# Performance work log

Hardware: AMD Instinct MI355X
Metric: run time of the kernel (lower is better)

## Reference

```python
import jax, jax.numpy as jnp
import numpy as np

D_MODEL = 1024
D_ATT = 1024
N_HEAD = 16
HEAD_DIM = D_ATT // N_HEAD


def setup_inputs() -> dict:
    key = jax.random.key(0)
    ks = jax.random.split(key, 9)
    s = 0.02
    return {
        "x": jax.random.normal(ks[0], (4, 2048, D_MODEL), dtype=jnp.float32),
        "Wq": jax.random.normal(ks[1], (D_MODEL, D_ATT), dtype=jnp.float32) * s,
        "bq": jnp.zeros((D_ATT,), dtype=jnp.float32),
        "Wk": jax.random.normal(ks[2], (D_MODEL, D_ATT), dtype=jnp.float32) * s,
        "bk": jnp.zeros((D_ATT,), dtype=jnp.float32),
        "Wv": jax.random.normal(ks[3], (D_MODEL, D_ATT), dtype=jnp.float32) * s,
        "bv": jnp.zeros((D_ATT,), dtype=jnp.float32),
        "Wp": jax.random.normal(ks[4], (D_ATT, D_MODEL), dtype=jnp.float32) * s,
        "bp": jnp.zeros((D_MODEL,), dtype=jnp.float32),
    }


def reference(x, Wq, bq, Wk, bk, Wv, bv, Wp, bp):
    B, T, C = x.shape
    # project and split heads: [B, H, T, Dh]
    q = (x @ Wq + bq).reshape(B, T, N_HEAD, HEAD_DIM).transpose(0, 2, 1, 3)
    k = (x @ Wk + bk).reshape(B, T, N_HEAD, HEAD_DIM).transpose(0, 2, 1, 3)
    v = (x @ Wv + bv).reshape(B, T, N_HEAD, HEAD_DIM).transpose(0, 2, 1, 3)
    scale = 1.0 / jnp.sqrt(jnp.float32(HEAD_DIM))
    att = jnp.einsum("bhqd,bhkd->bhqk", q, k) * scale
    causal = jnp.tril(jnp.ones((T, T), dtype=bool))
    att = jnp.where(causal, att, jnp.float32(-jnp.inf))
    att = jax.nn.softmax(att, axis=-1)
    y = jnp.einsum("bhqk,bhkd->bhqd", att, v)
    y = y.transpose(0, 2, 1, 3).reshape(B, T, D_ATT)
    return y @ Wp + bp
```

## Files before the change

kernel.cpp:

```cpp
#include <hip/hip_runtime.h>
#include <hip/hip_bf16.h>
#include <stdint.h>

#define TSEQ 2048
#define NB   4
#define NHEAD 16
#define HDIM 64
#define DM   1024
#define BTOT (NB*TSEQ)

typedef __attribute__((ext_vector_type(8))) short bf16x8;
typedef __attribute__((ext_vector_type(4))) float f32x4;
typedef __attribute__((ext_vector_type(16))) float f32x16;
typedef __attribute__((ext_vector_type(2))) unsigned u32x2;

__device__ __forceinline__ unsigned short f2bf(float f){
  union { float f; unsigned u; } v; v.f = f;
  unsigned r = v.u + 0x7fffu + ((v.u >> 16) & 1u);
  return (unsigned short)(r >> 16);
}

__device__ __forceinline__ unsigned cvt_pk_bf16(float lo, float hi){
  unsigned r;
  asm("v_cvt_pk_bf16_f32 %0, %1, %2" : "=v"(r) : "v"(lo), "v"(hi));
  return r;
}

__device__ __forceinline__ float exp2_raw(float x){
#if __has_builtin(__builtin_amdgcn_exp2f)
  return __builtin_amdgcn_exp2f(x);
#else
  return exp2f(x);
#endif
}

__device__ __forceinline__ u32x2 pl32swap(unsigned a, unsigned b){
  auto r = __builtin_amdgcn_permlane32_swap((int)a, (int)b, false, false);
  return (u32x2){(unsigned)r[0], (unsigned)r[1]};
}

__device__ __forceinline__ void gload_lds16(const void* g, void* l){
  __builtin_amdgcn_global_load_lds(
      (const __attribute__((address_space(1))) void*)g,
      (__attribute__((address_space(3))) void*)l,
      16, 0, 0);
}

__global__ __launch_bounds__(256) void k_prep(
    const float* __restrict__ x, unsigned short* __restrict__ x_bf,
    const float* __restrict__ Wq, const float* __restrict__ Wk,
    const float* __restrict__ Wv, const float* __restrict__ Wp,
    unsigned short* __restrict__ Wq_t, unsigned short* __restrict__ Wk_t,
    unsigned short* __restrict__ Wv_t, unsigned short* __restrict__ Wp_t)
{
  __shared__ unsigned short tile_s[32][33];
  const int bid = blockIdx.x;
  if (bid < 8192){
    size_t j = ((size_t)bid * 256 + threadIdx.x) * 4;
    float4 v = *reinterpret_cast<const float4*>(x + j);
    unsigned long long pk =  (unsigned long long)f2bf(v.x)
                          | ((unsigned long long)f2bf(v.y) << 16)
                          | ((unsigned long long)f2bf(v.z) << 32)
                          | ((unsigned long long)f2bf(v.w) << 48);
    *reinterpret_cast<unsigned long long*>(x_bf + j) = pk;
  } else {
    const int r   = bid - 8192;
    const int job = r >> 10, tile = r & 1023;
    const float* W = (job == 0) ? Wq : (job == 1) ? Wk : (job == 2) ? Wv : Wp;
    unsigned short* Wt = (job == 0) ? Wq_t : (job == 1) ? Wk_t : (job == 2) ? Wv_t : Wp_t;
    const int n0 = (tile & 31) * 32, k0 = (tile >> 5) * 32;
    const int tx = threadIdx.x & 31, ty = threadIdx.x >> 5;
    #pragma unroll
    for (int j = ty; j < 32; j += 8)
      tile_s[j][tx] = f2bf(W[(size_t)(k0 + j) * DM + n0 + tx]);
    __syncthreads();
    #pragma unroll
    for (int j = ty; j < 32; j += 8)
      Wt[(size_t)(n0 + j) * DM + k0 + tx] = tile_s[tx][j];
  }
}

template<int MODE, int BM, int BN, int WM, int WN>
__global__ __launch_bounds__(512) void k_gemm2(
    const unsigned short* __restrict__ A,
    const unsigned short* __restrict__ Bt,
    const float* __restrict__ bias,
    const float* __restrict__ bias2,
    void* __restrict__ out, int M, int N, int K, float oscale)
{
  constexpr int TM = BM / WM, TN = BN / WN;
  constexpr int MF = TM / 16, NF = TN / 16;
  constexpr int AH = BM / 2,  BH = BN / 2;
  __shared__ unsigned short As[2][2][AH * 64];
  __shared__ unsigned short Bs[2][2][BH * 64];

  const int t    = threadIdx.x;
  const int lane = t & 63;
  const int w    = t >> 6;
  const int wm   = w / WN;
  const int wn   = w % WN;
  const int lr   = lane & 15;
  const int ck   = lane >> 4;
  const int rb   = ck << 2;

  const int gx  = gridDim.x;
  const int nwg = gx * gridDim.y;
  const int lid = blockIdx.y * gx + blockIdx.x;
  const int swz = (lid & 7) * (nwg >> 3) + (lid >> 3);
  const int n0  = (swz % gx) * BN;
  const int m0  = (swz / gx) * BM;

  const int aHalf = (wm * TM) / AH, aBase = (wm * TM) % AH;
  const int bHalf = (wn * TN) / BH, bBase = (wn * TN) % BH;

  auto stgA = [&](int buf, int kt){
    #pragma unroll
    for (int ht = 0; ht < 2; ++ht)
      #pragma unroll
      for (int rr = 0; rr < AH / 64; ++rr){
        int u = t + rr * 512;
        int row = u >> 3, c = u & 7, cs = c ^ (row & 7);
        gload_lds16(A + (size_t)(m0 + ht * AH + row) * K + kt * 64 + cs * 8,
                    &As[buf][ht][u * 8]);
      }
  };
  auto stgB = [&](int buf, int kt){
    #pragma unroll
    for (int ht = 0; ht < 2; ++ht)
      #pragma unroll
      for (int rr = 0; rr < BH / 64; ++rr){
        int u = t + rr * 512;
        int row = u >> 3, c = u & 7, cs = c ^ (row & 7);
        gload_lds16(Bt + (size_t)(n0 + ht * BH + row) * K + kt * 64 + cs * 8,
                    &Bs[buf][ht][u * 8]);
      }
  };

  f32x4 acc[MF][NF];
  #pragma unroll
  for (int i = 0; i < MF; ++i)
    #pragma unroll
    for (int j = 0; j < NF; ++j) acc[i][j] = (f32x4){0.f, 0.f, 0.f, 0.f};

  const int NT = K >> 6;

  stgA(0, 0); stgB(0, 0);

  for (int kt = 0; kt < NT; ++kt){
    const int cur = kt & 1;
    const unsigned short* Ah = &As[cur][aHalf][0];
    const unsigned short* Bh = &Bs[cur][bHalf][0];

    if (kt + 1 < NT){
      stgA(cur ^ 1, kt + 1);
      asm volatile("s_waitcnt vmcnt(%0)" :: "n"(BM / 64) : "memory");
    } else {
      asm volatile("s_waitcnt vmcnt(0)" ::: "memory");
    }
    __builtin_amdgcn_s_barrier();
    __builtin_amdgcn_sched_barrier(0);
    {
      bf16x8 af[MF], bfr[NF];
      #pragma unroll
      for (int i = 0; i < MF; ++i)
        af[i]  = *reinterpret_cast<const bf16x8*>(&Ah[(aBase + i * 16 + lr) * 64 + (ck ^ (lr & 7)) * 8]);
      #pragma unroll
      for (int i = 0; i < NF; ++i)
        bfr[i] = *reinterpret_cast<const bf16x8*>(&Bh[(bBase + i * 16 + lr) * 64 + (ck ^ (lr & 7)) * 8]);
      __builtin_amdgcn_s_setprio(1);
      #pragma unroll
      for (int mi = 0; mi < MF; ++mi)
        #pragma unroll
        for (int ni = 0; ni < NF; ++ni)
          acc[mi][ni] = __builtin_amdgcn_mfma_f32_16x16x32_bf16(af[mi], bfr[ni], acc[mi][ni], 0, 0, 0);
      __builtin_amdgcn_s_setprio(0);
    }

    if (kt + 1 < NT) stgB(cur ^ 1, kt + 1);
    {
      bf16x8 af[MF], bfr[NF];
      #pragma unroll
      for (int i = 0; i < MF; ++i)
        af[i]  = *reinterpret_cast<const bf16x8*>(&Ah[(aBase + i * 16 + lr) * 64 + ((4 + ck) ^ (lr & 7)) * 8]);
      #pragma unroll
      for (int i = 0; i < NF; ++i)
        bfr[i] = *reinterpret_cast<const bf16x8*>(&Bh[(bBase + i * 16 + lr) * 64 + ((4 + ck) ^ (lr & 7)) * 8]);
      __builtin_amdgcn_s_setprio(1);
      #pragma unroll
      for (int mi = 0; mi < MF; ++mi)
        #pragma unroll
        for (int ni = 0; ni < NF; ++ni)
          acc[mi][ni] = __builtin_amdgcn_mfma_f32_16x16x32_bf16(af[mi], bfr[ni], acc[mi][ni], 0, 0, 0);
      __builtin_amdgcn_s_setprio(0);
    }
    __builtin_amdgcn_s_barrier();
  }

  #pragma unroll
  for (int mf = 0; mf < MF; ++mf){
    #pragma unroll
    for (int ni = 0; ni < NF; ++ni){
      #pragma unroll
      for (int r = 0; r < 4; ++r){
        int m = m0 + wm * TM + mf * 16 + rb + r;
        int n = n0 + wn * TN + ni * 16 + lr;
        float v = acc[mf][ni][r];
        if (MODE == 1){
          v = (v + bias[m]) * oscale;
          int b = n >> 11, tt = n & 2047, h = m >> 6, d = m & 63;
          ((unsigned short*)out)[(((size_t)(b * 16 + h) * 64 + d) << 11) + tt] = f2bf(v);
        } else if (MODE == 2){
          v += bias[n];
          ((float*)out)[(size_t)m * N + n] = v;
        } else {
          int seg = n >> 10, nn = n & 1023;
          v += seg ? bias2[nn] : bias[nn];
          if (!seg) v *= oscale;
          int b = m >> 11, tt = m & 2047, h = nn >> 6, d = nn & 63;
          ((unsigned short*)out)[(size_t)seg * BTOT * DM +
              (((size_t)(b * 16 + h) * 2048 + tt) << 6) + d] = f2bf(v);
        }
      }
    }
  }
}

#define ATTN_PV(OD, KB)                                                        \
  {                                                                            \
    unsigned pk0a = cvt_pk_bf16(p[0],  p[1]);                                  \
    unsigned pk0b = cvt_pk_bf16(p[2],  p[3]);                                  \
    unsigned pk1a = cvt_pk_bf16(p[4],  p[5]);                                  \
    unsigned pk1b = cvt_pk_bf16(p[6],  p[7]);                                  \
    unsigned pk2a = cvt_pk_bf16(p[8],  p[9]);                                  \
    unsigned pk2b = cvt_pk_bf16(p[10], p[11]);                                 \
    unsigned pk3a = cvt_pk_bf16(p[12], p[13]);                                 \
    unsigned pk3b = cvt_pk_bf16(p[14], p[15]);                                 \
    __builtin_amdgcn_s_setprio(1);                                             \
    {                                                                          \
      u32x2 r0 = pl32swap(pk0a, pk1a);                                         \
      u32x2 r1 = pl32swap(pk0b, pk1b);                                         \
      union { unsigned u[4]; bf16x8 v; } ap;                                   \
      ap.u[0] = r0[0]; ap.u[1] = r1[0]; ap.u[2] = r0[1]; ap.u[3] = r1[1];      \
      const int wg = (KB) * 2;                                                 \
      _Pragma("unroll")                                                        \
      for (int ntd = 0; ntd < 2; ++ntd){                                       \
        int row = ntd * 32 + l31;                                              \
        bf16x8 bV = *reinterpret_cast<const bf16x8*>(                          \
            &Vs[cur][row * 64 + ((2 * wg + c2) ^ (row & 7)) * 8]);             \
        OD[ntd] = __builtin_amdgcn_mfma_f32_32x32x16_bf16(ap.v, bV, OD[ntd], 0, 0, 0); \
      }                                                                        \
    }                                                                          \
    {                                                                          \
      u32x2 r0 = pl32swap(pk2a, pk3a);                                         \
      u32x2 r1 = pl32swap(pk2b, pk3b);                                         \
      union { unsigned u[4]; bf16x8 v; } ap;                                   \
      ap.u[0] = r0[0]; ap.u[1] = r1[0]; ap.u[2] = r0[1]; ap.u[3] = r1[1];      \
      const int wg = (KB) * 2 + 1;                                             \
      _Pragma("unroll")                                                        \
      for (int ntd = 0; ntd < 2; ++ntd){                                       \
        int row = ntd * 32 + l31;                                              \
        bf16x8 bV = *reinterpret_cast<const bf16x8*>(                          \
            &Vs[cur][row * 64 + ((2 * wg + c2) ^ (row & 7)) * 8]);             \
        OD[ntd] = __builtin_amdgcn_mfma_f32_32x32x16_bf16(ap.v, bV, OD[ntd], 0, 0, 0); \
      }                                                                        \
    }                                                                          \
    __builtin_amdgcn_s_setprio(0);                                             \
  }

#define ATTN_SUBTILE(OD, KB)                                                   \
  {                                                                            \
    const int kvb = kv0 + (KB) * 32;                                           \
    if (kvb <= wave_max){                                                      \
      f32x16 st = {};                                                          \
      __builtin_amdgcn_s_setprio(1);                                           \
      _Pragma("unroll")                                                        \
      for (int m = 0; m < 4; ++m){                                             \
        int row = (KB) * 32 + l31;                                             \
        bf16x8 aK = *reinterpret_cast<const bf16x8*>(                          \
            &Ks[cur][row * 64 + ((2 * m + c2) ^ (row & 7)) * 8]);              \
        st = __builtin_amdgcn_mfma_f32_32x32x16_bf16(aK, bQ[m], st, 0, 0, 0);  \
      }                                                                        \
      __builtin_amdgcn_s_setprio(0);                                           \
      const bool need_mask = (kvb + 31 > q0);                                  \
      float p[16];                                                             \
      _Pragma("unroll")                                                        \
      for (int rg = 0; rg < 16; ++rg){                                         \
        float pv = exp2_raw(st[rg]);                                           \
        if (need_mask){                                                        \
          int kv = kvb + 4 * c2 + 8 * (rg >> 2) + (rg & 3);                    \
          pv = (kv > qrow) ? 0.f : pv;                                         \
        }                                                                      \
        p[rg] = pv;                                                            \
      }                                                                        \
      {                                                                        \
        float s0 = (p[0] + p[1]) + (p[2] + p[3]);                              \
        float s1 = (p[4] + p[5]) + (p[6] + p[7]);                              \
        float s2 = (p[8] + p[9]) + (p[10] + p[11]);                            \
        float s3 = (p[12] + p[13]) + (p[14] + p[15]);                          \
        l_part += (s0 + s1) + (s2 + s3);                                       \
      }                                                                        \
      ATTN_PV(OD, KB)                                                          \
    }                                                                          \
  }

__global__ __launch_bounds__(512) void k_attn(
    const unsigned short* __restrict__ Qb,
    const unsigned short* __restrict__ Kb,
    const unsigned short* __restrict__ Vt,
    unsigned short* __restrict__ Ya)
{
  __shared__ unsigned short Ks[2][64 * 64];
  __shared__ unsigned short Vs[2][64 * 64];

  const int t    = threadIdx.x;
  const int lane = t & 63;
  const int w    = t >> 6;
  const int bh   = blockIdx.y;
  const int blk  = blockIdx.x;
  const int l31  = lane & 31;
  const int c2   = lane >> 5;

  const unsigned short* Qp = Qb + (size_t)bh * TSEQ * 64;
  const unsigned short* Kp = Kb + (size_t)bh * TSEQ * 64;
  const unsigned short* Vp = Vt + (size_t)bh * 64 * TSEQ;
  const int b = bh >> 4, h = bh & 15;

  const int qt   = (w >> 2) ? (15 - blk) : blk;
  const int q0   = qt * 128 + (w & 3) * 32;
  const int wave_max = q0 + 31;
  const int ntiles   = 2 * (15 - blk) + 2;
  const int qrow = q0 + l31;

  auto stage = [&](int buf, int kv0){
    int row = t >> 3, c = t & 7;
    int cs = c ^ (row & 7);
    gload_lds16(Kp + (size_t)(kv0 + row) * 64 + cs * 8, &Ks[buf][t * 8]);
    gload_lds16(Vp + (size_t)row * TSEQ + kv0 + cs * 8, &Vs[buf][t * 8]);
  };

  bf16x8 bQ[4];
  #pragma unroll
  for (int m = 0; m < 4; ++m)
    bQ[m] = *reinterpret_cast<const bf16x8*>(
        Qp + (size_t)qrow * 64 + m * 16 + c2 * 8);

  f32x16 oA[2] = {}, oB[2] = {};
  float l_part = 0.f;

  stage(0, 0);
  int cur = 0;

  for (int it = 0; it < ntiles; ++it){
    __builtin_amdgcn_sched_barrier(0);
    __builtin_amdgcn_s_barrier();
    if (it + 1 < ntiles){
      stage(cur ^ 1, (it + 1) * 64);
      asm volatile("s_waitcnt vmcnt(2)" ::: "memory");
    } else {
      asm volatile("s_waitcnt vmcnt(0)" ::: "memory");
    }
    __builtin_amdgcn_s_barrier();
    __builtin_amdgcn_sched_barrier(0);

    const int kv0 = it * 64;
    ATTN_SUBTILE(oA, 0)
    ATTN_SUBTILE(oB, 1)
    cur ^= 1;
  }

  float l_full = l_part + __shfl_xor(l_part, 32);
  float linv[16];
  #pragma unroll
  for (int rg = 0; rg < 16; ++rg){
    int qloc = 4 * c2 + 8 * (rg >> 2) + (rg & 3);
    linv[rg] = __builtin_amdgcn_rcpf(__shfl(l_full, qloc));
  }
  #pragma unroll
  for (int ntd = 0; ntd < 2; ++ntd)
    #pragma unroll
    for (int rg = 0; rg < 16; ++rg){
      int q = q0 + 4 * c2 + 8 * (rg >> 2) + (rg & 3);
      int d = ntd * 32 + l31;
      float v = (oA[ntd][rg] + oB[ntd][rg]) * linv[rg];
      Ya[((size_t)(b * 2048 + q)) * 1024 + h * 64 + d] = f2bf(v);
    }
}

extern "C" void kernel_launch(void* const* d_in, const int* in_sizes, int n_in,
                              void* d_out, int out_size, void* d_ws, size_t ws_size,
                              hipStream_t stream)
{
  const float* x  = (const float*)d_in[0];
  const float* Wq = (const float*)d_in[1];
  const float* bq = (const float*)d_in[2];
  const float* Wk = (const float*)d_in[3];
  const float* bk = (const float*)d_in[4];
  const float* Wv = (const float*)d_in[5];
  const float* bv = (const float*)d_in[6];
  const float* Wp = (const float*)d_in[7];
  const float* bp = (const float*)d_in[8];
  float* out = (float*)d_out;

  unsigned short* ws   = (unsigned short*)d_ws;
  unsigned short* x_bf = ws;
  unsigned short* Wq_t = x_bf + (size_t)BTOT * DM;
  unsigned short* Wk_t = Wq_t + (size_t)DM * DM;
  unsigned short* Wv_t = Wk_t + (size_t)DM * DM;
  unsigned short* Wp_t = Wv_t + (size_t)DM * DM;
  unsigned short* Qb   = Wp_t + (size_t)DM * DM;
  unsigned short* Kb   = Qb   + (size_t)BTOT * DM;
  unsigned short* Vt   = Kb   + (size_t)BTOT * DM;
  unsigned short* Ya   = Vt   + (size_t)BTOT * DM;

  const float QSCALE = 0.125f * 1.44269504f;

  k_prep<<<8192 + 4096, 256, 0, stream>>>(
      x, x_bf, Wq, Wk, Wv, Wp, Wq_t, Wk_t, Wv_t, Wp_t);

  k_gemm2<3, 256, 256, 2, 4><<<dim3(2048 / 256, BTOT / 256), 512, 0, stream>>>(
      x_bf, Wq_t, bq, bk, Qb, BTOT, 2048, DM, QSCALE);
  k_gemm2<1, 128, 256, 2, 4><<<dim3(BTOT / 256, DM / 128), 512, 0, stream>>>(
      Wv_t, x_bf, bv, nullptr, Vt, DM, BTOT, DM, 1.0f);

  k_attn<<<dim3(8, NB * NHEAD), 512, 0, stream>>>(Qb, Kb, Vt, Ya);

  k_gemm2<2, 256, 128, 4, 2><<<dim3(DM / 128, BTOT / 256), 512, 0, stream>>>(
      Ya, Wp_t, bp, nullptr, out, BTOT, DM, DM, 1.0f);
}
```

Measured before the change: 180.2 us.

## Split GEMM k-step into four half-M phases with interleaved loads and barriers

Restructures the GEMM main loop into four phases, each handling half the M fragments for one k-half. LDS fragment reads, global-to-LDS prefetch issue, and barriers are interleaved between the MFMA blocks so waves stay in lockstep and memory work overlaps compute, in the style of ping-pong scheduling. The wait for the next tile moves to the end of the iteration, and an explicit wait plus barrier is added before the loop. It adds more barriers per iteration, which costs synchronization overhead if the waves do not overlap well, and halves the A-fragment register footprint.

```diff
diff --git a/kernel.cpp b/kernel.cpp
--- a/kernel.cpp
+++ b/kernel.cpp
@@ -90,6 +90,7 @@
 {
   constexpr int TM = BM / WM, TN = BN / WN;
   constexpr int MF = TM / 16, NF = TN / 16;
+  constexpr int MH = MF / 2;
   constexpr int AH = BM / 2,  BH = BN / 2;
   __shared__ unsigned short As[2][2][AH * 64];
   __shared__ unsigned short Bs[2][2][BH * 64];
@@ -145,54 +146,82 @@
   const int NT = K >> 6;
 
   stgA(0, 0); stgB(0, 0);
+  asm volatile("s_waitcnt vmcnt(0)" ::: "memory");
+  __builtin_amdgcn_s_barrier();
 
   for (int kt = 0; kt < NT; ++kt){
     const int cur = kt & 1;
     const unsigned short* Ah = &As[cur][aHalf][0];
     const unsigned short* Bh = &Bs[cur][bHalf][0];
-
-    if (kt + 1 < NT){
-      stgA(cur ^ 1, kt + 1);
-      asm volatile("s_waitcnt vmcnt(%0)" :: "n"(BM / 64) : "memory");
-    } else {
-      asm volatile("s_waitcnt vmcnt(0)" ::: "memory");
-    }
-    __builtin_amdgcn_s_barrier();
-    __builtin_amdgcn_sched_barrier(0);
-    {
-      bf16x8 af[MF], bfr[NF];
-      #pragma unroll
-      for (int i = 0; i < MF; ++i)
-        af[i]  = *reinterpret_cast<const bf16x8*>(&Ah[(aBase + i * 16 + lr) * 64 + (ck ^ (lr & 7)) * 8]);
-      #pragma unroll
-      for (int i = 0; i < NF; ++i)
-        bfr[i] = *reinterpret_cast<const bf16x8*>(&Bh[(bBase + i * 16 + lr) * 64 + (ck ^ (lr & 7)) * 8]);
-      __builtin_amdgcn_s_setprio(1);
-      #pragma unroll
-      for (int mi = 0; mi < MF; ++mi)
-        #pragma unroll
-        for (int ni = 0; ni < NF; ++ni)
-          acc[mi][ni] = __builtin_amdgcn_mfma_f32_16x16x32_bf16(af[mi], bfr[ni], acc[mi][ni], 0, 0, 0);
-      __builtin_amdgcn_s_setprio(0);
-    }
-
+    bf16x8 af[MH], bfr[NF];
+
+    #pragma unroll
+    for (int i = 0; i < MH; ++i)
+      af[i]  = *reinterpret_cast<const bf16x8*>(&Ah[(aBase + i * 16 + lr) * 64 + (ck ^ (lr & 7)) * 8]);
+    #pragma unroll
+    for (int i = 0; i < NF; ++i)
+      bfr[i] = *reinterpret_cast<const bf16x8*>(&Bh[(bBase + i * 16 + lr) * 64 + (ck ^ (lr & 7)) * 8]);
+    if (kt + 1 < NT) stgA(cur ^ 1, kt + 1);
+    __builtin_amdgcn_s_barrier();
+    asm volatile("s_waitcnt lgkmcnt(0)" ::: "memory");
+    __builtin_amdgcn_sched_barrier(0);
+    __builtin_amdgcn_s_setprio(1);
+    #pragma unroll
+    for (int mi = 0; mi < MH; ++mi)
+      #pragma unroll
+      for (int ni = 0; ni < NF; ++ni)
+        acc[mi][ni] = __builtin_amdgcn_mfma_f32_16x16x32_bf16(af[mi], bfr[ni], acc[mi][ni], 0, 0, 0);
+    __builtin_amdgcn_s_setprio(0);
+    __builtin_amdgcn_s_barrier();
+
+    #pragma unroll
+    for (int i = 0; i < MH; ++i)
+      af[i]  = *reinterpret_cast<const bf16x8*>(&Ah[(aBase + (MH + i) * 16 + lr) * 64 + (ck ^ (lr & 7)) * 8]);
     if (kt + 1 < NT) stgB(cur ^ 1, kt + 1);
-    {
-      bf16x8 af[MF], bfr[NF];
-      #pragma unroll
-      for (int i = 0; i < MF; ++i)
-        af[i]  = *reinterpret_cast<const bf16x8*>(&Ah[(aBase + i * 16 + lr) * 64 + ((4 + ck) ^ (lr & 7)) * 8]);
-      #pragma unroll
-      for (int i = 0; i < NF; ++i)
-        bfr[i] = *reinterpret_cast<const bf16x8*>(&Bh[(bBase + i * 16 + lr) * 64 + ((4 + ck) ^ (lr & 7)) * 8]);
-      __builtin_amdgcn_s_setprio(1);
-      #pragma unroll
-      for (int mi = 0; mi < MF; ++mi)
-        #pragma unroll
-        for (int ni = 0; ni < NF; ++ni)
-          acc[mi][ni] = __builtin_amdgcn_mfma_f32_16x16x32_bf16(af[mi], bfr[ni], acc[mi][ni], 0, 0, 0);
-      __builtin_amdgcn_s_setprio(0);
-    }
+    __builtin_amdgcn_s_barrier();
+    asm volatile("s_waitcnt lgkmcnt(0)" ::: "memory");
+    __builtin_amdgcn_sched_barrier(0);
+    __builtin_amdgcn_s_setprio(1);
+    #pragma unroll
+    for (int mi = 0; mi < MH; ++mi)
+      #pragma unroll
+      for (int ni = 0; ni < NF; ++ni)
+        acc[MH + mi][ni] = __builtin_amdgcn_mfma_f32_16x16x32_bf16(af[mi], bfr[ni], acc[MH + mi][ni], 0, 0, 0);
+    __builtin_amdgcn_s_setprio(0);
+    __builtin_amdgcn_s_barrier();
+
+    #pragma unroll
+    for (int i = 0; i < MH; ++i)
+      af[i]  = *reinterpret_cast<const bf16x8*>(&Ah[(aBase + i * 16 + lr) * 64 + ((4 + ck) ^ (lr & 7)) * 8]);
+    #pragma unroll
+    for (int i = 0; i < NF; ++i)
+      bfr[i] = *reinterpret_cast<const bf16x8*>(&Bh[(bBase + i * 16 + lr) * 64 + ((4 + ck) ^ (lr & 7)) * 8]);
+    __builtin_amdgcn_s_barrier();
+    asm volatile("s_waitcnt lgkmcnt(0)" ::: "memory");
+    __builtin_amdgcn_sched_barrier(0);
+    __builtin_amdgcn_s_setprio(1);
+    #pragma unroll
+    for (int mi = 0; mi < MH; ++mi)
+      #pragma unroll
+      for (int ni = 0; ni < NF; ++ni)
+        acc[mi][ni] = __builtin_amdgcn_mfma_f32_16x16x32_bf16(af[mi], bfr[ni], acc[mi][ni], 0, 0, 0);
+    __builtin_amdgcn_s_setprio(0);
+    __builtin_amdgcn_s_barrier();
+
+    #pragma unroll
+    for (int i = 0; i < MH; ++i)
+      af[i]  = *reinterpret_cast<const bf16x8*>(&Ah[(aBase + (MH + i) * 16 + lr) * 64 + ((4 + ck) ^ (lr & 7)) * 8]);
+    __builtin_amdgcn_s_barrier();
+    asm volatile("s_waitcnt lgkmcnt(0)" ::: "memory");
+    __builtin_amdgcn_sched_barrier(0);
+    __builtin_amdgcn_s_setprio(1);
+    #pragma unroll
+    for (int mi = 0; mi < MH; ++mi)
+      #pragma unroll
+      for (int ni = 0; ni < NF; ++ni)
+        acc[MH + mi][ni] = __builtin_amdgcn_mfma_f32_16x16x32_bf16(af[mi], bfr[ni], acc[MH + mi][ni], 0, 0, 0);
+    __builtin_amdgcn_s_setprio(0);
+    asm volatile("s_waitcnt vmcnt(0)" ::: "memory");
     __builtin_amdgcn_s_barrier();
   }
 
```

Result: faster. 175.1 us (-2.9%).
